# Kernel optimization log

Hardware: AMD Instinct MI355X
Metric: run time of the kernel (lower is better)

Reference implementation:

```python
import jax, jax.numpy as jnp
import numpy as np
import math

B, T, D = 2, 2048, 2048
N_HEADS, N_KV_HEADS = 16, 4
HEAD_DIM = D // N_HEADS          # 128
N_GROUPS = N_HEADS // N_KV_HEADS # 4


def setup_inputs() -> dict:
    key = jax.random.key(0)
    k1, k2, k3, k4, k5 = jax.random.split(key, 5)
    x = jax.random.normal(k1, (B, T, D), dtype=jnp.float32)
    # RoPE table: [T, head_dim//2, 2] = (cos, sin)
    inv_freq = 1.0 / (10000.0 ** (np.arange(0, HEAD_DIM, 2, dtype=np.float32) / HEAD_DIM))
    ang = np.arange(T, dtype=np.float32)[:, None] * inv_freq[None, :]  # [T, hd/2]
    rope = jnp.asarray(np.stack([np.cos(ang), np.sin(ang)], axis=-1), dtype=jnp.float32)
    s = 0.02
    wq = s * jax.random.normal(k2, (N_HEADS * HEAD_DIM, D), dtype=jnp.float32)
    wk = s * jax.random.normal(k3, (N_KV_HEADS * HEAD_DIM, D), dtype=jnp.float32)
    wv = s * jax.random.normal(k4, (N_KV_HEADS * HEAD_DIM, D), dtype=jnp.float32)
    wo = s * jax.random.normal(k5, (D, D), dtype=jnp.float32)
    return {"x": x, "rope": rope, "wq": wq, "wk": wk, "wv": wv, "wo": wo}


def apply_rope(t, rope):
    # t: [B, H, T, hd]; rope: [T, hd/2, 2]
    d = t.shape[-1]
    t1, t2 = t[..., : d // 2], t[..., d // 2 :]
    cos = rope[..., 0][None, None]  # [1,1,T,hd/2]
    sin = rope[..., 1][None, None]
    return jnp.concatenate([t1 * cos - t2 * sin, t1 * sin + t2 * cos], axis=-1)


def reference(x, rope, wq, wk, wv, wo):
    b, t, c = x.shape
    q = (x @ wq.T).reshape(b, t, N_HEADS, HEAD_DIM).transpose(0, 2, 1, 3)
    k = (x @ wk.T).reshape(b, t, N_KV_HEADS, HEAD_DIM).transpose(0, 2, 1, 3)
    v = (x @ wv.T).reshape(b, t, N_KV_HEADS, HEAD_DIM).transpose(0, 2, 1, 3)
    q = apply_rope(q, rope)
    k = apply_rope(k, rope)
    k = jnp.repeat(k, N_GROUPS, axis=1)  # [B, H, T, hd]
    v = jnp.repeat(v, N_GROUPS, axis=1)
    scale = 1.0 / math.sqrt(HEAD_DIM)
    scores = jnp.einsum("bhqd,bhkd->bhqk", q, k) * scale
    causal = jnp.tril(jnp.ones((t, t), dtype=bool))
    scores = jnp.where(causal[None, None], scores, jnp.finfo(scores.dtype).min)
    attn = jax.nn.softmax(scores, axis=-1)
    y = jnp.einsum("bhqk,bhkd->bhqd", attn, v)
    y = y.transpose(0, 2, 1, 3).reshape(b, t, c)
    return y @ wo.T
```

## Files before the change

### kernel.cpp

```cpp
#include <hip/hip_runtime.h>

typedef unsigned short u16;
typedef float   f32x4  __attribute__((ext_vector_type(4)));
typedef short   short8 __attribute__((ext_vector_type(8)));
typedef __bf16  bf16x8 __attribute__((ext_vector_type(8)));
typedef float   float4v __attribute__((ext_vector_type(4)));
typedef unsigned short u16x4 __attribute__((ext_vector_type(4)));

static __device__ __forceinline__ u16 f2b(float f) {
  return __builtin_bit_cast(u16, (__bf16)f);
}
static __device__ __forceinline__ float b2f(u16 h) {
  union { unsigned u; float f; } v; v.u = ((unsigned)h) << 16;
  return v.f;
}
static __device__ __forceinline__ f32x4 mfma_bf16(short8 a, short8 b, f32x4 c) {
  return __builtin_amdgcn_mfma_f32_16x16x32_bf16(
      __builtin_bit_cast(bf16x8, a), __builtin_bit_cast(bf16x8, b), c, 0, 0, 0);
}
static __device__ __forceinline__ void gload_lds16(const u16* g, u16* l) {
  __builtin_amdgcn_global_load_lds(
      (const __attribute__((address_space(1))) unsigned int*)g,
      (__attribute__((address_space(3))) unsigned int*)l, 16, 0, 0);
}

#define BB 2
#define TT 2048
#define DD 2048
#define NH 16
#define NKVH 4
#define HD 128
#define MM (BB * TT)
#define QSTR 3072
#define QSCALE 0.08838834764831845f

#define N4_X   ((MM * DD) / 4)
#define N4_WQ  ((DD * DD) / 4)
#define N4_WKV ((NKVH * HD * DD) / 4)
#define N4_WO  ((DD * DD) / 4)
#define N4_TOT (N4_X + N4_WQ + 2 * N4_WKV + N4_WO)

__global__ __launch_bounds__(256) void cvt_all(const float* __restrict__ x,
                                               const float* __restrict__ wq,
                                               const float* __restrict__ wk,
                                               const float* __restrict__ wv,
                                               const float* __restrict__ wo,
                                               u16* __restrict__ xb,
                                               u16* __restrict__ wqkvb,
                                               u16* __restrict__ wob) {
  int stride = gridDim.x * blockDim.x;
  for (int i = blockIdx.x * blockDim.x + threadIdx.x; i < N4_TOT; i += stride) {
    const float4v* src;
    u16x4* dst;
    int off;
    if (i < N4_X) {
      src = (const float4v*)x; dst = (u16x4*)xb; off = i;
    } else if (i < N4_X + N4_WQ) {
      src = (const float4v*)wq; dst = (u16x4*)wqkvb; off = i - N4_X;
    } else if (i < N4_X + N4_WQ + N4_WKV) {
      src = (const float4v*)wk; dst = (u16x4*)wqkvb + N4_WQ; off = i - (N4_X + N4_WQ);
    } else if (i < N4_X + N4_WQ + 2 * N4_WKV) {
      src = (const float4v*)wv; dst = (u16x4*)wqkvb + N4_WQ + N4_WKV;
      off = i - (N4_X + N4_WQ + N4_WKV);
    } else {
      src = (const float4v*)wo; dst = (u16x4*)wob; off = i - (N4_X + N4_WQ + 2 * N4_WKV);
    }
    float4v v = src[off];
    u16x4 o;
    o[0] = f2b(v[0]); o[1] = f2b(v[1]); o[2] = f2b(v[2]); o[3] = f2b(v[3]);
    dst[off] = o;
  }
}

__global__ __launch_bounds__(256) void rope_k(u16* __restrict__ K,
                                              const float* __restrict__ rope) {
  int idx = blockIdx.x * 256 + threadIdx.x;
  int i  = idx & 63;
  int h  = (idx >> 6) & (NKVH - 1);
  int bt = idx >> 8;
  int t  = bt & (TT - 1);
  size_t base = (size_t)bt * QSTR + h * HD + i;
  float x1 = b2f(K[base]);
  float x2 = b2f(K[base + 64]);
  float c = rope[t * 128 + 2 * i];
  float s = rope[t * 128 + 2 * i + 1];
  K[base]      = f2b(x1 * c - x2 * s);
  K[base + 64] = f2b(x1 * s + x2 * c);
}

__global__ __launch_bounds__(512) void gemm_qkv(const u16* __restrict__ A,
                                                const u16* __restrict__ W,
                                                u16* __restrict__ C,
                                                int M, int N, int K) {
  __shared__ __align__(16) u16 As[2][2][128 * 64];
  __shared__ __align__(16) u16 Ws[2][192 * 64];

  const int tid = threadIdx.x, lane = tid & 63, wid = tid >> 6;
  const int wm = wid >> 2, wn = wid & 3;
  const int l15 = lane & 15, lh = lane >> 4;

  const int nwg = gridDim.x * gridDim.y;
  const int lin = blockIdx.y * gridDim.x + blockIdx.x;
  const int swz = (lin & 7) * (nwg >> 3) + (lin >> 3);
  const int brow = (swz / gridDim.x) * 256, bcol = (swz % gridDim.x) * 192;

  const int srp = wid * 8 + (lane >> 3);
  const int gsw = ((lane & 7) ^ (lane >> 3)) << 3;
  const u16* sa[2][2];
  const u16* sw3[3];
#pragma unroll
  for (int mh = 0; mh < 2; ++mh)
#pragma unroll
    for (int i = 0; i < 2; ++i)
      sa[mh][i] = A + (size_t)(brow + mh * 128 + i * 64 + srp) * K + gsw;
#pragma unroll
  for (int i = 0; i < 3; ++i)
    sw3[i] = W + (size_t)(bcol + i * 64 + srp) * K + gsw;

  f32x4 acc[8][3];
#pragma unroll
  for (int mi = 0; mi < 8; ++mi)
#pragma unroll
    for (int ni = 0; ni < 3; ++ni) acc[mi][ni] = (f32x4)0.0f;

  const int nk = K >> 6;

  auto issue = [&](int t, int p) {
#pragma unroll
    for (int mh = 0; mh < 2; ++mh)
#pragma unroll
      for (int i = 0; i < 2; ++i)
        gload_lds16(sa[mh][i] + t * 64, &As[p][mh][i * 4096 + wid * 512]);
#pragma unroll
    for (int i = 0; i < 3; ++i)
      gload_lds16(sw3[i] + t * 64, &Ws[p][i * 4096 + wid * 512]);
  };

  issue(0, 0);
  for (int t = 0; t < nk; ++t) {
    const int p = t & 1;
    if (t + 1 < nk) {
      issue(t + 1, p ^ 1);
      asm volatile("s_waitcnt vmcnt(7)" ::: "memory");
    } else {
      asm volatile("s_waitcnt vmcnt(0)" ::: "memory");
    }
    __builtin_amdgcn_sched_barrier(0);
    __builtin_amdgcn_s_barrier();
    __builtin_amdgcn_sched_barrier(0);

    const u16* Ab = &As[p][wm][0];
    const u16* Wb = &Ws[p][0];

    short8 af[4][2], bf[3][2];
#pragma unroll
    for (int ni = 0; ni < 3; ++ni)
#pragma unroll
      for (int ks = 0; ks < 2; ++ks) {
        int rh = wn * 48 + ni * 16 + l15;
        bf[ni][ks] = *(const short8*)&Wb[rh * 64 + (((ks * 4 + lh) ^ (rh & 7)) << 3)];
      }
#pragma unroll
    for (int mi = 0; mi < 4; ++mi)
#pragma unroll
      for (int ks = 0; ks < 2; ++ks) {
        int rh = mi * 16 + l15;
        af[mi][ks] = *(const short8*)&Ab[rh * 64 + (((ks * 4 + lh) ^ (rh & 7)) << 3)];
      }
    __builtin_amdgcn_s_setprio(1);
#pragma unroll
    for (int mi = 0; mi < 4; ++mi)
#pragma unroll
      for (int ni = 0; ni < 3; ++ni)
#pragma unroll
        for (int ks = 0; ks < 2; ++ks)
          acc[mi][ni] = mfma_bf16(af[mi][ks], bf[ni][ks], acc[mi][ni]);
    __builtin_amdgcn_s_setprio(0);
#pragma unroll
    for (int mi = 0; mi < 4; ++mi)
#pragma unroll
      for (int ks = 0; ks < 2; ++ks) {
        int rh = (4 + mi) * 16 + l15;
        af[mi][ks] = *(const short8*)&Ab[rh * 64 + (((ks * 4 + lh) ^ (rh & 7)) << 3)];
      }
    __builtin_amdgcn_s_setprio(1);
#pragma unroll
    for (int mi = 0; mi < 4; ++mi)
#pragma unroll
      for (int ni = 0; ni < 3; ++ni)
#pragma unroll
        for (int ks = 0; ks < 2; ++ks)
          acc[4 + mi][ni] = mfma_bf16(af[mi][ks], bf[ni][ks], acc[4 + mi][ni]);
    __builtin_amdgcn_s_setprio(0);

    asm volatile("s_waitcnt lgkmcnt(0)" ::: "memory");
    __builtin_amdgcn_sched_barrier(0);
    __builtin_amdgcn_s_barrier();
    __builtin_amdgcn_sched_barrier(0);
  }

#pragma unroll
  for (int mi = 0; mi < 8; ++mi)
#pragma unroll
    for (int ni = 0; ni < 3; ++ni)
#pragma unroll
      for (int j = 0; j < 4; ++j) {
        int row = brow + wm * 128 + mi * 16 + lh * 4 + j;
        int col = bcol + wn * 48 + ni * 16 + l15;
        C[(size_t)row * N + col] = f2b(acc[mi][ni][j]);
      }
}

__global__ __launch_bounds__(512, 2) void gemm_wo(const u16* __restrict__ A,
                                                  const u16* __restrict__ W,
                                                  float* __restrict__ C,
                                                  int M, int N, int K) {
  __shared__ __align__(16) u16 As[2][2][128 * 64];
  __shared__ __align__(16) u16 Ws[2][128 * 64];

  const int tid = threadIdx.x, lane = tid & 63, wid = tid >> 6;
  const int wm = wid >> 2, wn = wid & 3;
  const int l15 = lane & 15, lh = lane >> 4;

  const int nwg = gridDim.x * gridDim.y;
  const int lin = blockIdx.y * gridDim.x + blockIdx.x;
  const int swz = (lin & 7) * (nwg >> 3) + (lin >> 3);
  const int brow = (swz / gridDim.x) * 256, bcol = (swz % gridDim.x) * 128;

  const int srp = wid * 8 + (lane >> 3);
  const int gsw = ((lane & 7) ^ (lane >> 3)) << 3;
  const u16* sa[2][2];
  const u16* sw2[2];
#pragma unroll
  for (int mh = 0; mh < 2; ++mh)
#pragma unroll
    for (int i = 0; i < 2; ++i)
      sa[mh][i] = A + (size_t)(brow + mh * 128 + i * 64 + srp) * K + gsw;
#pragma unroll
  for (int i = 0; i < 2; ++i)
    sw2[i] = W + (size_t)(bcol + i * 64 + srp) * K + gsw;

  f32x4 acc[8][2];
#pragma unroll
  for (int mi = 0; mi < 8; ++mi)
#pragma unroll
    for (int ni = 0; ni < 2; ++ni) acc[mi][ni] = (f32x4)0.0f;

  const int nk = K >> 6;

  auto issue = [&](int t, int p) {
#pragma unroll
    for (int mh = 0; mh < 2; ++mh)
#pragma unroll
      for (int i = 0; i < 2; ++i)
        gload_lds16(sa[mh][i] + t * 64, &As[p][mh][i * 4096 + wid * 512]);
#pragma unroll
    for (int i = 0; i < 2; ++i)
      gload_lds16(sw2[i] + t * 64, &Ws[p][i * 4096 + wid * 512]);
  };

  issue(0, 0);
  for (int t = 0; t < nk; ++t) {
    const int p = t & 1;
    if (t + 1 < nk) {
      issue(t + 1, p ^ 1);
      asm volatile("s_waitcnt vmcnt(6)" ::: "memory");
    } else {
      asm volatile("s_waitcnt vmcnt(0)" ::: "memory");
    }
    __builtin_amdgcn_sched_barrier(0);
    __builtin_amdgcn_s_barrier();
    __builtin_amdgcn_sched_barrier(0);

    const u16* Ab = &As[p][wm][0];
    const u16* Wb = &Ws[p][0];

    short8 af[4][2], bf[2][2];
#pragma unroll
    for (int ni = 0; ni < 2; ++ni)
#pragma unroll
      for (int ks = 0; ks < 2; ++ks) {
        int rh = wn * 32 + ni * 16 + l15;
        bf[ni][ks] = *(const short8*)&Wb[rh * 64 + (((ks * 4 + lh) ^ (rh & 7)) << 3)];
      }
#pragma unroll
    for (int mi = 0; mi < 4; ++mi)
#pragma unroll
      for (int ks = 0; ks < 2; ++ks) {
        int rh = mi * 16 + l15;
        af[mi][ks] = *(const short8*)&Ab[rh * 64 + (((ks * 4 + lh) ^ (rh & 7)) << 3)];
      }
    __builtin_amdgcn_s_setprio(1);
#pragma unroll
    for (int mi = 0; mi < 4; ++mi)
#pragma unroll
      for (int ni = 0; ni < 2; ++ni)
#pragma unroll
        for (int ks = 0; ks < 2; ++ks)
          acc[mi][ni] = mfma_bf16(af[mi][ks], bf[ni][ks], acc[mi][ni]);
    __builtin_amdgcn_s_setprio(0);
#pragma unroll
    for (int mi = 0; mi < 4; ++mi)
#pragma unroll
      for (int ks = 0; ks < 2; ++ks) {
        int rh = (4 + mi) * 16 + l15;
        af[mi][ks] = *(const short8*)&Ab[rh * 64 + (((ks * 4 + lh) ^ (rh & 7)) << 3)];
      }
    __builtin_amdgcn_s_setprio(1);
#pragma unroll
    for (int mi = 0; mi < 4; ++mi)
#pragma unroll
      for (int ni = 0; ni < 2; ++ni)
#pragma unroll
        for (int ks = 0; ks < 2; ++ks)
          acc[4 + mi][ni] = mfma_bf16(af[mi][ks], bf[ni][ks], acc[4 + mi][ni]);
    __builtin_amdgcn_s_setprio(0);

    asm volatile("s_waitcnt lgkmcnt(0)" ::: "memory");
    __builtin_amdgcn_sched_barrier(0);
    __builtin_amdgcn_s_barrier();
    __builtin_amdgcn_sched_barrier(0);
  }

#pragma unroll
  for (int mi = 0; mi < 8; ++mi)
#pragma unroll
    for (int ni = 0; ni < 2; ++ni)
#pragma unroll
      for (int j = 0; j < 4; ++j) {
        int row = brow + wm * 128 + mi * 16 + lh * 4 + j;
        int col = bcol + wn * 32 + ni * 16 + l15;
        C[(size_t)row * N + col] = acc[mi][ni][j];
      }
}

#define QBLK 128
#define KVBLK 128

static __device__ __forceinline__ void attn_tile(
    const short8* qa, f32x4* o, float& l, float& m,
    int qrow0, int kv0,
    const u16* Ks, const unsigned* Vt32, u16* myP,
    int l15, int lh) {
  if (kv0 > qrow0 + 15) return;

  f32x4 st[4];
#pragma unroll
  for (int nt = 0; nt < 4; ++nt) st[nt] = (f32x4)0.0f;
  __builtin_amdgcn_s_setprio(1);
#pragma unroll
  for (int nt = 0; nt < 4; ++nt) {
    const u16* krow = &Ks[(nt * 16 + l15) * 136 + (lh << 3)];
#pragma unroll
    for (int kk = 0; kk < 4; ++kk) {
      short8 kb = *(const short8*)(krow + kk * 32);
      st[nt] = mfma_bf16(kb, qa[kk], st[nt]);
    }
  }
  __builtin_amdgcn_s_setprio(0);

  const int kvq = kv0 + lh * 4 - qrow0 - l15;
#pragma unroll
  for (int nt = 0; nt < 4; ++nt)
#pragma unroll
    for (int j = 0; j < 4; ++j)
      if (kvq + nt * 16 + j > 0) st[nt][j] = -1e30f;

  float mt = st[0][0];
#pragma unroll
  for (int nt = 0; nt < 4; ++nt)
#pragma unroll
    for (int j = 0; j < 4; ++j) mt = fmaxf(mt, st[nt][j]);
  mt = fmaxf(mt, __shfl_xor(mt, 16));
  mt = fmaxf(mt, __shfl_xor(mt, 32));

  if (!__all(mt - m <= 8.0f)) {
    float mn = fmaxf(m, mt);
    float a = __expf(m - mn);
    m = mn;
    l *= a;
    float aj[4];
#pragma unroll
    for (int j = 0; j < 4; ++j) aj[j] = __shfl(a, lh * 4 + j);
#pragma unroll
    for (int n = 0; n < 8; ++n)
#pragma unroll
      for (int j = 0; j < 4; ++j) o[n][j] *= aj[j];
  }

  f32x4 p[4];
  float ps = 0.0f;
#pragma unroll
  for (int nt = 0; nt < 4; ++nt) {
#pragma unroll
    for (int j = 0; j < 4; ++j) p[nt][j] = __expf(st[nt][j] - m);
    ps += (p[nt][0] + p[nt][1]) + (p[nt][2] + p[nt][3]);
  }
  l += ps;

  unsigned* P32 = (unsigned*)myP;
  const int pb = l15 * 36 + lh * 2;
#pragma unroll
  for (int nt = 0; nt < 4; ++nt)
#pragma unroll
    for (int jj = 0; jj < 2; ++jj)
      P32[pb + nt * 8 + jj] =
          (unsigned)f2b(p[nt][2 * jj]) | ((unsigned)f2b(p[nt][2 * jj + 1]) << 16);

  __builtin_amdgcn_s_setprio(1);
#pragma unroll
  for (int c = 0; c < 2; ++c) {
    short8 pa = *(const short8*)&myP[l15 * 72 + c * 32 + (lh << 3)];
#pragma unroll
    for (int nt2 = 0; nt2 < 8; ++nt2) {
      int d = nt2 * 16 + l15;
      int byteoff = (d * 144 + (c * 32 + lh * 8) * 2) ^ (((d >> 3) & 7) << 4);
      short8 vb = *(const short8*)((const char*)Vt32 + byteoff);
      o[nt2] = mfma_bf16(pa, vb, o[nt2]);
    }
  }
  __builtin_amdgcn_s_setprio(0);
}

__global__ __launch_bounds__(512) void attn_kernel(const u16* __restrict__ QKV,
                                                   const float* __restrict__ rope,
                                                   u16* __restrict__ Y) {
  __shared__ __align__(16) u16 Ks[2][64 * 136];
  __shared__ __align__(16) unsigned Vt32[2][128 * 36];
  __shared__ __align__(16) u16 Ps[8][16 * 72];

  const int tid = threadIdx.x, lane = tid & 63, wid = tid >> 6;
  const int l15 = lane & 15, lh = lane >> 4;
  const int bid = blockIdx.x;
  const int qpair = bid & 7;
  const int h = (bid >> 3) & 15;
  const int b = bid >> 7;
  const int kvh = h >> 2;
  const int qtA = qpair, qtB = 15 - qpair;
  const int rowA = qtA * QBLK + wid * 16;
  const int rowB = qtB * QBLK + wid * 16;

  const u16* Kb_ = QKV + (size_t)b * TT * QSTR + DD + kvh * HD;
  const u16* Vb_ = Kb_ + NKVH * HD;

  short8 qaA[4], qaB[4];
  {
    const u16* qA = QKV + (size_t)(b * TT + rowA + l15) * QSTR + h * HD + (lh << 3);
    const u16* qB = QKV + (size_t)(b * TT + rowB + l15) * QSTR + h * HD + (lh << 3);
#pragma unroll
    for (int kk = 0; kk < 4; ++kk) {
      qaA[kk] = *(const short8*)(qA + kk * 32);
      qaB[kk] = *(const short8*)(qB + kk * 32);
    }
  }
  {
    const float* rpA = rope + (size_t)(rowA + l15) * 128;
    const float* rpB = rope + (size_t)(rowB + l15) * 128;
#pragma unroll
    for (int kk = 0; kk < 2; ++kk)
#pragma unroll
      for (int e = 0; e < 8; ++e) {
        const int i2 = 2 * (kk * 32 + (lh << 3) + e);
        float c = rpA[i2], s = rpA[i2 + 1];
        float x1 = b2f((u16)qaA[kk][e]), x2 = b2f((u16)qaA[kk + 2][e]);
        qaA[kk][e]     = (short)f2b(QSCALE * (x1 * c - x2 * s));
        qaA[kk + 2][e] = (short)f2b(QSCALE * (x1 * s + x2 * c));
        float cb = rpB[i2], sb = rpB[i2 + 1];
        float y1 = b2f((u16)qaB[kk][e]), y2 = b2f((u16)qaB[kk + 2][e]);
        qaB[kk][e]     = (short)f2b(QSCALE * (y1 * cb - y2 * sb));
        qaB[kk + 2][e] = (short)f2b(QSCALE * (y1 * sb + y2 * cb));
      }
  }

  f32x4 oA[8], oB[8];
  float lA = 0.0f, lB = 0.0f;
  float mA = -1e30f, mB = -1e30f;
#pragma unroll
  for (int n = 0; n < 8; ++n) { oA[n] = (f32x4)0.0f; oB[n] = (f32x4)0.0f; }

  const int kvend = (qtB + 1) * QBLK;

  short8 kreg[4], vreg[4];
  const int srow = tid >> 4;
  const int sc8 = (tid & 15) << 3;

  auto issue = [&](int kv0) {
    kreg[0] = *(const short8*)&Kb_[(size_t)(kv0 + srow) * QSTR + sc8];
    kreg[1] = *(const short8*)&Kb_[(size_t)(kv0 + 32 + srow) * QSTR + sc8];
    kreg[2] = *(const short8*)&Kb_[(size_t)(kv0 + 64 + srow) * QSTR + sc8];
    kreg[3] = *(const short8*)&Kb_[(size_t)(kv0 + 96 + srow) * QSTR + sc8];
    vreg[0] = *(const short8*)&Vb_[(size_t)(kv0 + 2 * srow) * QSTR + sc8];
    vreg[1] = *(const short8*)&Vb_[(size_t)(kv0 + 2 * srow + 1) * QSTR + sc8];
    vreg[2] = *(const short8*)&Vb_[(size_t)(kv0 + 64 + 2 * srow) * QSTR + sc8];
    vreg[3] = *(const short8*)&Vb_[(size_t)(kv0 + 64 + 2 * srow + 1) * QSTR + sc8];
  };

  issue(0);
  for (int kv0 = 0; kv0 < kvend; kv0 += KVBLK) {
    __syncthreads();
    *(short8*)&Ks[0][srow * 136 + sc8] = kreg[0];
    *(short8*)&Ks[0][(srow + 32) * 136 + sc8] = kreg[1];
    *(short8*)&Ks[1][srow * 136 + sc8] = kreg[2];
    *(short8*)&Ks[1][(srow + 32) * 136 + sc8] = kreg[3];
#pragma unroll
    for (int e = 0; e < 8; ++e) {
      int d = sc8 + e;
      unsigned pk0 = (unsigned)(u16)vreg[0][e] | ((unsigned)(u16)vreg[1][e] << 16);
      unsigned pk1 = (unsigned)(u16)vreg[2][e] | ((unsigned)(u16)vreg[3][e] << 16);
      int byteoff = (d * 144 + 4 * srow) ^ (((d >> 3) & 7) << 4);
      *(unsigned*)((char*)&Vt32[0][0] + byteoff) = pk0;
      *(unsigned*)((char*)&Vt32[1][0] + byteoff) = pk1;
    }
    __syncthreads();
    if (kv0 + KVBLK < kvend) issue(kv0 + KVBLK);

    attn_tile(qaA, oA, lA, mA, rowA, kv0,      &Ks[0][0], &Vt32[0][0], &Ps[wid][0], l15, lh);
    attn_tile(qaA, oA, lA, mA, rowA, kv0 + 64, &Ks[1][0], &Vt32[1][0], &Ps[wid][0], l15, lh);
    attn_tile(qaB, oB, lB, mB, rowB, kv0,      &Ks[0][0], &Vt32[0][0], &Ps[wid][0], l15, lh);
    attn_tile(qaB, oB, lB, mB, rowB, kv0 + 64, &Ks[1][0], &Vt32[1][0], &Ps[wid][0], l15, lh);
  }

  lA += __shfl_xor(lA, 16); lA += __shfl_xor(lA, 32);
  lB += __shfl_xor(lB, 16); lB += __shfl_xor(lB, 32);
  f32x4 invA, invB;
#pragma unroll
  for (int j = 0; j < 4; ++j) {
    invA[j] = __builtin_amdgcn_rcpf(__shfl(lA, lh * 4 + j));
    invB[j] = __builtin_amdgcn_rcpf(__shfl(lB, lh * 4 + j));
  }
#pragma unroll
  for (int nt = 0; nt < 8; ++nt)
#pragma unroll
    for (int j = 0; j < 4; ++j) {
      Y[(size_t)(b * TT + rowA + lh * 4 + j) * DD + h * HD + nt * 16 + l15] =
          f2b(oA[nt][j] * invA[j]);
      Y[(size_t)(b * TT + rowB + lh * 4 + j) * DD + h * HD + nt * 16 + l15] =
          f2b(oB[nt][j] * invB[j]);
    }
}

extern "C" void kernel_launch(void* const* d_in, const int* in_sizes, int n_in,
                              void* d_out, int out_size, void* d_ws, size_t ws_size,
                              hipStream_t stream) {
  const float* x    = (const float*)d_in[0];
  const float* rope = (const float*)d_in[1];
  const float* wq   = (const float*)d_in[2];
  const float* wk   = (const float*)d_in[3];
  const float* wv   = (const float*)d_in[4];
  const float* wo   = (const float*)d_in[5];
  float* out = (float*)d_out;

  char* ws = (char*)d_ws;
  u16* xb    = (u16*)ws; ws += (size_t)MM * DD * 2;
  u16* wqkvb = (u16*)ws; ws += (size_t)QSTR * DD * 2;
  u16* wob   = (u16*)ws; ws += (size_t)DD * DD * 2;
  u16* QKVb  = (u16*)ws; ws += (size_t)MM * QSTR * 2;
  u16* Yb    = (u16*)ws;

  cvt_all<<<2048, 256, 0, stream>>>(x, wq, wk, wv, wo, xb, wqkvb, wob);

  gemm_qkv<<<dim3(QSTR / 192, MM / 256), 512, 0, stream>>>(xb, wqkvb, QKVb, MM, QSTR, DD);

  rope_k<<<(MM * NKVH * 64) / 256, 256, 0, stream>>>(QKVb + DD, rope);

  attn_kernel<<<BB * NH * (TT / QBLK / 2), 512, 0, stream>>>(QKVb, rope, Yb);

  gemm_wo<<<dim3(DD / 128, MM / 256), 512, 0, stream>>>(Yb, wob, out, MM, DD, DD);
}
```

Before: 198.4 us.

## Double-buffer K/V tiles with direct-to-LDS K loads and XOR swizzle

K tiles are now loaded straight from global memory into LDS with global_load_lds into an XOR-swizzled, unpadded layout instead of going through registers. K and V shared buffers are double-buffered, so the next tile's loads are issued before the current tile's compute and V is written to the alternate buffer afterwards, leaving one barrier per iteration. The aim is to hide global latency behind MFMA work and to free the K staging registers. The cost is twice the LDS (about 130KB), which may limit occupancy, and there is no explicit vmcnt wait before the barrier for the asynchronous LDS loads.

New measurement: 202.8 us. 1.02x slower.

```diff
diff --git a/kernel.cpp b/kernel.cpp
--- a/kernel.cpp
+++ b/kernel.cpp
@@ -350,10 +350,10 @@
   __builtin_amdgcn_s_setprio(1);
 #pragma unroll
   for (int nt = 0; nt < 4; ++nt) {
-    const u16* krow = &Ks[(nt * 16 + l15) * 136 + (lh << 3)];
+    const u16* krow = &Ks[(nt * 16 + l15) * 128];
 #pragma unroll
     for (int kk = 0; kk < 4; ++kk) {
-      short8 kb = *(const short8*)(krow + kk * 32);
+      short8 kb = *(const short8*)(krow + ((((kk << 2) + lh) ^ (l15 & 7)) << 3));
       st[nt] = mfma_bf16(kb, qa[kk], st[nt]);
     }
   }
@@ -425,8 +425,8 @@
 __global__ __launch_bounds__(512) void attn_kernel(const u16* __restrict__ QKV,
                                                    const float* __restrict__ rope,
                                                    u16* __restrict__ Y) {
-  __shared__ __align__(16) u16 Ks[2][64 * 136];
-  __shared__ __align__(16) unsigned Vt32[2][128 * 36];
+  __shared__ __align__(16) u16 Ksw[2][2][64 * 128];
+  __shared__ __align__(16) unsigned V32[2][2][128 * 36];
   __shared__ __align__(16) u16 Ps[8][16 * 72];
 
   const int tid = threadIdx.x, lane = tid & 63, wid = tid >> 6;
@@ -480,44 +480,60 @@
 
   const int kvend = (qtB + 1) * QBLK;
 
-  short8 kreg[4], vreg[4];
+  short8 vreg[4];
   const int srow = tid >> 4;
   const int sc8 = (tid & 15) << 3;
 
-  auto issue = [&](int kv0) {
-    kreg[0] = *(const short8*)&Kb_[(size_t)(kv0 + srow) * QSTR + sc8];
-    kreg[1] = *(const short8*)&Kb_[(size_t)(kv0 + 32 + srow) * QSTR + sc8];
-    kreg[2] = *(const short8*)&Kb_[(size_t)(kv0 + 64 + srow) * QSTR + sc8];
-    kreg[3] = *(const short8*)&Kb_[(size_t)(kv0 + 96 + srow) * QSTR + sc8];
+  auto issueK = [&](int kv0, int pb) {
+#pragma unroll
+    for (int s = 0; s < 2; ++s)
+#pragma unroll
+      for (int j = 0; j < 2; ++j) {
+        const int rr = wid * 8 + j * 4 + (lane >> 4);
+        const int cs = ((lane & 15) ^ (rr & 7)) << 3;
+        gload_lds16(Kb_ + (size_t)(kv0 + s * 64 + rr) * QSTR + cs,
+                    &Ksw[pb][s][wid * 1024 + j * 512]);
+      }
+  };
+  auto loadV = [&](int kv0) {
     vreg[0] = *(const short8*)&Vb_[(size_t)(kv0 + 2 * srow) * QSTR + sc8];
     vreg[1] = *(const short8*)&Vb_[(size_t)(kv0 + 2 * srow + 1) * QSTR + sc8];
     vreg[2] = *(const short8*)&Vb_[(size_t)(kv0 + 64 + 2 * srow) * QSTR + sc8];
     vreg[3] = *(const short8*)&Vb_[(size_t)(kv0 + 64 + 2 * srow + 1) * QSTR + sc8];
   };
-
-  issue(0);
-  for (int kv0 = 0; kv0 < kvend; kv0 += KVBLK) {
-    __syncthreads();
-    *(short8*)&Ks[0][srow * 136 + sc8] = kreg[0];
-    *(short8*)&Ks[0][(srow + 32) * 136 + sc8] = kreg[1];
-    *(short8*)&Ks[1][srow * 136 + sc8] = kreg[2];
-    *(short8*)&Ks[1][(srow + 32) * 136 + sc8] = kreg[3];
+  auto writeV = [&](int pb) {
 #pragma unroll
     for (int e = 0; e < 8; ++e) {
       int d = sc8 + e;
       unsigned pk0 = (unsigned)(u16)vreg[0][e] | ((unsigned)(u16)vreg[1][e] << 16);
       unsigned pk1 = (unsigned)(u16)vreg[2][e] | ((unsigned)(u16)vreg[3][e] << 16);
       int byteoff = (d * 144 + 4 * srow) ^ (((d >> 3) & 7) << 4);
-      *(unsigned*)((char*)&Vt32[0][0] + byteoff) = pk0;
-      *(unsigned*)((char*)&Vt32[1][0] + byteoff) = pk1;
-    }
+      *(unsigned*)((char*)&V32[pb][0][0] + byteoff) = pk0;
+      *(unsigned*)((char*)&V32[pb][1][0] + byteoff) = pk1;
+    }
+  };
+
+  issueK(0, 0);
+  loadV(0);
+  writeV(0);
+  __syncthreads();
+
+  int p = 0;
+  for (int kv0 = 0; kv0 < kvend; kv0 += KVBLK) {
+    const bool more = (kv0 + KVBLK < kvend);
+    if (more) {
+      issueK(kv0 + KVBLK, p ^ 1);
+      loadV(kv0 + KVBLK);
+    }
+
+    attn_tile(qaA, oA, lA, mA, rowA, kv0,      &Ksw[p][0][0], &V32[p][0][0], &Ps[wid][0], l15, lh);
+    attn_tile(qaA, oA, lA, mA, rowA, kv0 + 64, &Ksw[p][1][0], &V32[p][1][0], &Ps[wid][0], l15, lh);
+    attn_tile(qaB, oB, lB, mB, rowB, kv0,      &Ksw[p][0][0], &V32[p][0][0], &Ps[wid][0], l15, lh);
+    attn_tile(qaB, oB, lB, mB, rowB, kv0 + 64, &Ksw[p][1][0], &V32[p][1][0], &Ps[wid][0], l15, lh);
+
+    if (more) writeV(p ^ 1);
     __syncthreads();
-    if (kv0 + KVBLK < kvend) issue(kv0 + KVBLK);
-
-    attn_tile(qaA, oA, lA, mA, rowA, kv0,      &Ks[0][0], &Vt32[0][0], &Ps[wid][0], l15, lh);
-    attn_tile(qaA, oA, lA, mA, rowA, kv0 + 64, &Ks[1][0], &Vt32[1][0], &Ps[wid][0], l15, lh);
-    attn_tile(qaB, oB, lB, mB, rowB, kv0,      &Ks[0][0], &Vt32[0][0], &Ps[wid][0], l15, lh);
-    attn_tile(qaB, oB, lB, mB, rowB, kv0 + 64, &Ks[1][0], &Vt32[1][0], &Ps[wid][0], l15, lh);
+    p ^= 1;
   }
 
   lA += __shfl_xor(lA, 16); lA += __shfl_xor(lA, 32);
```

## Fuse fp32-to-bf16 conversion of x into the QKV GEMM A-tile load

Applied to the files above, without the earlier changes.

The separate conversion pass over the activation x is removed. The QKV GEMM now loads fp32 x straight into registers, converts it to bf16 and writes it to LDS, while the weight tiles still use direct global-to-LDS loads. This saves a full read-write round trip of the bf16 copy of x and shrinks the workspace. In exchange, the GEMM reads twice as many bytes for A from global memory, and every output-column tile re-reads that A. It also adds register pressure and extra waits on the LDS-store path.

Result: slower. 202.9 us (+2.3%).

```diff
diff --git a/kernel.cpp b/kernel.cpp
--- a/kernel.cpp
+++ b/kernel.cpp
@@ -34,36 +34,31 @@
 #define QSTR 3072
 #define QSCALE 0.08838834764831845f
 
-#define N4_X   ((MM * DD) / 4)
 #define N4_WQ  ((DD * DD) / 4)
 #define N4_WKV ((NKVH * HD * DD) / 4)
 #define N4_WO  ((DD * DD) / 4)
-#define N4_TOT (N4_X + N4_WQ + 2 * N4_WKV + N4_WO)
-
-__global__ __launch_bounds__(256) void cvt_all(const float* __restrict__ x,
-                                               const float* __restrict__ wq,
-                                               const float* __restrict__ wk,
-                                               const float* __restrict__ wv,
-                                               const float* __restrict__ wo,
-                                               u16* __restrict__ xb,
-                                               u16* __restrict__ wqkvb,
-                                               u16* __restrict__ wob) {
+#define N4W_TOT (N4_WQ + 2 * N4_WKV + N4_WO)
+
+__global__ __launch_bounds__(256) void cvt_w(const float* __restrict__ wq,
+                                             const float* __restrict__ wk,
+                                             const float* __restrict__ wv,
+                                             const float* __restrict__ wo,
+                                             u16* __restrict__ wqkvb,
+                                             u16* __restrict__ wob) {
   int stride = gridDim.x * blockDim.x;
-  for (int i = blockIdx.x * blockDim.x + threadIdx.x; i < N4_TOT; i += stride) {
+  for (int i = blockIdx.x * blockDim.x + threadIdx.x; i < N4W_TOT; i += stride) {
     const float4v* src;
     u16x4* dst;
     int off;
-    if (i < N4_X) {
-      src = (const float4v*)x; dst = (u16x4*)xb; off = i;
-    } else if (i < N4_X + N4_WQ) {
-      src = (const float4v*)wq; dst = (u16x4*)wqkvb; off = i - N4_X;
-    } else if (i < N4_X + N4_WQ + N4_WKV) {
-      src = (const float4v*)wk; dst = (u16x4*)wqkvb + N4_WQ; off = i - (N4_X + N4_WQ);
-    } else if (i < N4_X + N4_WQ + 2 * N4_WKV) {
+    if (i < N4_WQ) {
+      src = (const float4v*)wq; dst = (u16x4*)wqkvb; off = i;
+    } else if (i < N4_WQ + N4_WKV) {
+      src = (const float4v*)wk; dst = (u16x4*)wqkvb + N4_WQ; off = i - N4_WQ;
+    } else if (i < N4_WQ + 2 * N4_WKV) {
       src = (const float4v*)wv; dst = (u16x4*)wqkvb + N4_WQ + N4_WKV;
-      off = i - (N4_X + N4_WQ + N4_WKV);
+      off = i - (N4_WQ + N4_WKV);
     } else {
-      src = (const float4v*)wo; dst = (u16x4*)wob; off = i - (N4_X + N4_WQ + 2 * N4_WKV);
+      src = (const float4v*)wo; dst = (u16x4*)wob; off = i - (N4_WQ + 2 * N4_WKV);
     }
     float4v v = src[off];
     u16x4 o;
@@ -88,7 +83,7 @@
   K[base + 64] = f2b(x1 * s + x2 * c);
 }
 
-__global__ __launch_bounds__(512) void gemm_qkv(const u16* __restrict__ A,
+__global__ __launch_bounds__(512) void gemm_qkv(const float* __restrict__ X,
                                                 const u16* __restrict__ W,
                                                 u16* __restrict__ C,
                                                 int M, int N, int K) {
@@ -106,13 +101,13 @@
 
   const int srp = wid * 8 + (lane >> 3);
   const int gsw = ((lane & 7) ^ (lane >> 3)) << 3;
-  const u16* sa[2][2];
+  const float* xa[2][2];
   const u16* sw3[3];
 #pragma unroll
   for (int mh = 0; mh < 2; ++mh)
 #pragma unroll
     for (int i = 0; i < 2; ++i)
-      sa[mh][i] = A + (size_t)(brow + mh * 128 + i * 64 + srp) * K + gsw;
+      xa[mh][i] = X + (size_t)(brow + mh * 128 + i * 64 + srp) * K + gsw;
 #pragma unroll
   for (int i = 0; i < 3; ++i)
     sw3[i] = W + (size_t)(bcol + i * 64 + srp) * K + gsw;
@@ -125,26 +120,52 @@
 
   const int nk = K >> 6;
 
-  auto issue = [&](int t, int p) {
+  float4v areg[4][2];
+  auto loadA = [&](int t) {
 #pragma unroll
     for (int mh = 0; mh < 2; ++mh)
 #pragma unroll
-      for (int i = 0; i < 2; ++i)
-        gload_lds16(sa[mh][i] + t * 64, &As[p][mh][i * 4096 + wid * 512]);
+      for (int i = 0; i < 2; ++i) {
+        const float* s = xa[mh][i] + t * 64;
+        areg[mh * 2 + i][0] = *(const float4v*)(s);
+        areg[mh * 2 + i][1] = *(const float4v*)(s + 4);
+      }
+  };
+  auto writeA = [&](int p) {
+#pragma unroll
+    for (int mh = 0; mh < 2; ++mh)
+#pragma unroll
+      for (int i = 0; i < 2; ++i) {
+        short8 o;
+#pragma unroll
+        for (int e = 0; e < 4; ++e) {
+          o[e]     = (short)f2b(areg[mh * 2 + i][0][e]);
+          o[4 + e] = (short)f2b(areg[mh * 2 + i][1][e]);
+        }
+        *(short8*)&As[p][mh][i * 4096 + wid * 512 + lane * 8] = o;
+      }
+  };
+  auto issueW = [&](int t, int p) {
 #pragma unroll
     for (int i = 0; i < 3; ++i)
       gload_lds16(sw3[i] + t * 64, &Ws[p][i * 4096 + wid * 512]);
   };
 
-  issue(0, 0);
+  loadA(0);
+  issueW(0, 0);
+  asm volatile("s_waitcnt vmcnt(3)" ::: "memory");
+  writeA(0);
+
   for (int t = 0; t < nk; ++t) {
     const int p = t & 1;
     if (t + 1 < nk) {
-      issue(t + 1, p ^ 1);
-      asm volatile("s_waitcnt vmcnt(7)" ::: "memory");
+      loadA(t + 1);
+      issueW(t + 1, p ^ 1);
+      asm volatile("s_waitcnt vmcnt(11)" ::: "memory");
     } else {
       asm volatile("s_waitcnt vmcnt(0)" ::: "memory");
     }
+    asm volatile("s_waitcnt lgkmcnt(0)" ::: "memory");
     __builtin_amdgcn_sched_barrier(0);
     __builtin_amdgcn_s_barrier();
     __builtin_amdgcn_sched_barrier(0);
@@ -197,6 +218,10 @@
     __builtin_amdgcn_sched_barrier(0);
     __builtin_amdgcn_s_barrier();
     __builtin_amdgcn_sched_barrier(0);
+    if (t + 1 < nk) {
+      asm volatile("s_waitcnt vmcnt(3)" ::: "memory");
+      writeA(p ^ 1);
+    }
   }
 
 #pragma unroll
@@ -551,15 +576,14 @@
   float* out = (float*)d_out;
 
   char* ws = (char*)d_ws;
-  u16* xb    = (u16*)ws; ws += (size_t)MM * DD * 2;
   u16* wqkvb = (u16*)ws; ws += (size_t)QSTR * DD * 2;
   u16* wob   = (u16*)ws; ws += (size_t)DD * DD * 2;
   u16* QKVb  = (u16*)ws; ws += (size_t)MM * QSTR * 2;
   u16* Yb    = (u16*)ws;
 
-  cvt_all<<<2048, 256, 0, stream>>>(x, wq, wk, wv, wo, xb, wqkvb, wob);
-
-  gemm_qkv<<<dim3(QSTR / 192, MM / 256), 512, 0, stream>>>(xb, wqkvb, QKVb, MM, QSTR, DD);
+  cvt_w<<<2048, 256, 0, stream>>>(wq, wk, wv, wo, wqkvb, wob);
+
+  gemm_qkv<<<dim3(QSTR / 192, MM / 256), 512, 0, stream>>>(x, wqkvb, QKVb, MM, QSTR, DD);
 
   rope_k<<<(MM * NKVH * 64) / 256, 256, 0, stream>>>(QKVb + DD, rope);
 
```
